# Kernel tuning notes

Measured on AMD Instinct MI355X. Metric: run time of the kernel, lower is better.

## Reference

```python
import jax, jax.numpy as jnp
import numpy as np

B, C_IN, H_IMG, W_IMG = 8, 3, 512, 512
PATCH, EMBED, HEADS = 16, 768, 8
N = (H_IMG // PATCH) * (W_IMG // PATCH)  # 1024 patches per branch
OUT_DIM = H_IMG * W_IMG * C_IN // (N * 2)  # 384


def conv2d(x, w, b, stride):
    y = jax.lax.conv_general_dilated(x, w, (stride, stride), 'VALID',
                                     dimension_numbers=('NCHW', 'OIHW', 'NCHW'))
    return y + b[None, :, None, None]


def maxpool2(x):
    return jax.lax.reduce_window(x, -jnp.inf, jax.lax.max, (1, 1, 2, 2), (1, 1, 2, 2), 'VALID')


def patch_embed(x, w, b, pos):
    # conv stride=patch -> (B, E, H/p, W/p) -> (B, N, E) + pos
    y = conv2d(x, w, b, PATCH)
    Bc, E, Hp, Wp = y.shape
    return y.reshape(Bc, E, Hp * Wp).transpose(0, 2, 1) + pos


def bilinear_up_ac(x, s):
    # bilinear upsample, align_corners=True, separable along H then W
    Bc, Cc, H, W = x.shape
    ys = jnp.linspace(0.0, H - 1.0, H * s)
    y0 = jnp.floor(ys).astype(jnp.int32)
    y1 = jnp.minimum(y0 + 1, H - 1)
    wy = (ys - y0.astype(x.dtype))[:, None]  # (Ho,1)
    xh = x[:, :, y0, :] * (1.0 - wy) + x[:, :, y1, :] * wy
    xs = jnp.linspace(0.0, W - 1.0, W * s)
    x0 = jnp.floor(xs).astype(jnp.int32)
    x1 = jnp.minimum(x0 + 1, W - 1)
    wx = xs - x0.astype(x.dtype)
    return xh[:, :, :, x0] * (1.0 - wx) + xh[:, :, :, x1] * wx


def setup_inputs() -> dict:
    key = jax.random.key(0)
    ks = jax.random.split(key, 13)
    std = 0.02
    return {
        'img': jax.random.normal(ks[0], (B, C_IN, H_IMG, W_IMG), jnp.float32),
        'context': jax.random.normal(ks[1], (B, C_IN, 2 * H_IMG, 2 * W_IMG), jnp.float32),
        'patch_w': jax.random.normal(ks[2], (EMBED, C_IN, PATCH, PATCH), jnp.float32) * std,
        'patch_b': jax.random.normal(ks[3], (EMBED,), jnp.float32) * std,
        'pos1': jax.random.normal(ks[4], (1, N, EMBED), jnp.float32) * std,
        'ctx_w': jax.random.normal(ks[5], (EMBED, C_IN, PATCH, PATCH), jnp.float32) * std,
        'ctx_b': jax.random.normal(ks[6], (EMBED,), jnp.float32) * std,
        'pos2': jax.random.normal(ks[7], (1, N, EMBED), jnp.float32) * std,
        'qkv_w': jax.random.normal(ks[8], (EMBED, 3 * EMBED), jnp.float32) * std,
        'proj_w': jax.random.normal(ks[9], (EMBED, OUT_DIM), jnp.float32) * std,
        'proj_b': jax.random.normal(ks[10], (OUT_DIM,), jnp.float32) * std,
        'up_w': jax.random.normal(ks[11], (C_IN, C_IN, 1, 1), jnp.float32) * std,
        'up_b': jax.random.normal(ks[12], (C_IN,), jnp.float32) * std,
    }


def reference(img, context, patch_w, patch_b, pos1, ctx_w, ctx_b, pos2,
              qkv_w, proj_w, proj_b, up_w, up_b):
    # patch embeddings
    x = patch_embed(img, patch_w, patch_b, pos1)                    # (B, N, E)
    ce = patch_embed(maxpool2(context), ctx_w, ctx_b, pos2)          # (B, N, E)
    # cross attention (naive, faithful to torch module incl. scale quirk)
    xc = jnp.concatenate([x, ce], axis=1)                            # (B, 2N, E)
    qkv = xc @ qkv_w                                                 # (B, 2N, 3E)
    hd2 = 2 * EMBED // HEADS                                         # 192 per head
    qkv = qkv.reshape(B, N, 3, HEADS, hd2).transpose(2, 0, 3, 1, 4)  # (3, B, H, N, 192)
    q, k, v = qkv[0], qkv[1], qkv[2]
    scale = (EMBED // HEADS) ** -0.5                                 # 96**-0.5 quirk
    attn = jax.nn.softmax(jnp.einsum('bhnd,bhmd->bhnm', q, k) * scale, axis=-1)
    o = jnp.einsum('bhnm,bhmd->bhnd', attn, v)                       # (B, H, N, 192)
    o = o.transpose(0, 2, 1, 3).reshape(B, 2 * N, EMBED)
    o = o @ proj_w + proj_b                                          # (B, 2N, 384)
    # reshape to image, 1x1 conv, bilinear x2 (align_corners), sigmoid, gate
    y = o.reshape(B, C_IN, H_IMG, W_IMG)
    y = conv2d(y, up_w, up_b, 1)
    y = jax.nn.sigmoid(bilinear_up_ac(y, 2))
    y = y * context
    return (y, attn)
```

## Files before the change

### kernel.cpp

```cpp
#include <hip/hip_runtime.h>
#include <math.h>


namespace {

typedef unsigned short u16;
typedef __attribute__((ext_vector_type(8))) __bf16 bf16x8;
typedef __attribute__((ext_vector_type(4))) float f32x4;

constexpr float SCALE = 0.10206207261596577f;

__device__ __forceinline__ u16 f2bf(float x) {
  unsigned u = __float_as_uint(x);
  return (u16)((u + 0x7FFFu + ((u >> 16) & 1u)) >> 16);
}

template <int BM, int BN>
__device__ __forceinline__ void mfma_core(const u16* __restrict__ A, int lda, int m0,
                                          const u16* __restrict__ B, int ldb, int n0,
                                          int K, u16* As, u16* Bs,
                                          f32x4 (&acc)[BM / 32][BN / 32]) {
  const int tid = threadIdx.x;
  const int lane = tid & 63, wid = tid >> 6;
  const int wr = wid >> 1, wc = wid & 1;
  const int fr = lane & 15, ks = lane >> 4;
  const int srow = lane >> 2, sslot = lane & 3;
  for (int kc = 0; kc < K; kc += 32) {
#pragma unroll
    for (int t = 0; t < BM / 64; ++t) {
      const int rb = (wid * (BM / 64) + t) * 16;
      const u16* src = A + (size_t)(m0 + rb + srow) * lda + kc + sslot * 8;
      __builtin_amdgcn_global_load_lds((const __attribute__((address_space(1))) void*)src,
                                       (__attribute__((address_space(3))) void*)(As + rb * 32),
                                       16, 0, 0);
    }
#pragma unroll
    for (int t = 0; t < BN / 64; ++t) {
      const int rb = (wid * (BN / 64) + t) * 16;
      const u16* src = B + (size_t)(n0 + rb + srow) * ldb + kc + sslot * 8;
      __builtin_amdgcn_global_load_lds((const __attribute__((address_space(1))) void*)src,
                                       (__attribute__((address_space(3))) void*)(Bs + rb * 32),
                                       16, 0, 0);
    }
    __syncthreads();
    bf16x8 a[BM / 32], b[BN / 32];
#pragma unroll
    for (int mi = 0; mi < BM / 32; ++mi)
      a[mi] = *(const bf16x8*)(As + (wr * (BM / 2) + mi * 16 + fr) * 32 + ks * 8);
#pragma unroll
    for (int ni = 0; ni < BN / 32; ++ni)
      b[ni] = *(const bf16x8*)(Bs + (wc * (BN / 2) + ni * 16 + fr) * 32 + ks * 8);
#pragma unroll
    for (int mi = 0; mi < BM / 32; ++mi)
#pragma unroll
      for (int ni = 0; ni < BN / 32; ++ni)
        acc[mi][ni] = __builtin_amdgcn_mfma_f32_16x16x32_bf16(a[mi], b[ni], acc[mi][ni], 0, 0, 0);
    __syncthreads();
  }
}


__global__ void cvt_bf16(const float* __restrict__ in, u16* __restrict__ out) {
  const int i = blockIdx.x * 256 + threadIdx.x;
  const float4 v = ((const float4*)in)[i];
  ((ushort4*)out)[i] = make_ushort4(f2bf(v.x), f2bf(v.y), f2bf(v.z), f2bf(v.w));
}

__global__ void cvt_t(const float* __restrict__ in, u16* __restrict__ out, int N, int K) {
  __shared__ float t[32][33];
  const int tx = threadIdx.x, ty = threadIdx.y;
  const int bn = blockIdx.x * 32, bk = blockIdx.y * 32;
#pragma unroll
  for (int i = 0; i < 4; ++i) t[ty * 4 + i][tx] = in[(size_t)(bk + ty * 4 + i) * N + bn + tx];
  __syncthreads();
#pragma unroll
  for (int i = 0; i < 4; ++i)
    out[(size_t)(bn + ty * 4 + i) * K + bk + tx] = f2bf(t[tx][ty * 4 + i]);
}


__global__ void im2col_img(const float* __restrict__ img, u16* __restrict__ A) {
  const int t = threadIdx.x;
  const int row = blockIdx.x;
  const int k4 = t * 4;
  const int c = k4 >> 8, rem = k4 & 255, i = rem >> 4, j = rem & 15;
  const int b = row >> 10, n = row & 1023;
  const int hp = n >> 5, wp = n & 31;
  const float4 v = *(const float4*)(img + ((size_t)(b * 3 + c) * 512 + hp * 16 + i) * 512 + wp * 16 + j);
  *(ushort4*)(A + (size_t)row * 768 + k4) = make_ushort4(f2bf(v.x), f2bf(v.y), f2bf(v.z), f2bf(v.w));
}

__global__ void im2col_ctx(const float* __restrict__ ctx, u16* __restrict__ A) {
  const int t = threadIdx.x;
  const int row = blockIdx.x;
  const int k4 = t * 4;
  const int c = k4 >> 8, rem = k4 & 255, i = rem >> 4, j = rem & 15;
  const int b = row >> 10, n = row & 1023;
  const int hp = n >> 5, wp = n & 31;
  const int y = hp * 16 + i, x = wp * 16 + j;
  const float* base = ctx + ((size_t)(b * 3 + c) * 1024 + 2 * y) * 1024 + 2 * x;
  const float4 r0a = *(const float4*)(base);
  const float4 r0b = *(const float4*)(base + 4);
  const float4 r1a = *(const float4*)(base + 1024);
  const float4 r1b = *(const float4*)(base + 1028);
  *(ushort4*)(A + (size_t)row * 768 + k4) = make_ushort4(
      f2bf(fmaxf(fmaxf(r0a.x, r0a.y), fmaxf(r1a.x, r1a.y))),
      f2bf(fmaxf(fmaxf(r0a.z, r0a.w), fmaxf(r1a.z, r1a.w))),
      f2bf(fmaxf(fmaxf(r0b.x, r0b.y), fmaxf(r1b.x, r1b.y))),
      f2bf(fmaxf(fmaxf(r0b.z, r0b.w), fmaxf(r1b.z, r1b.w))));
}


__global__ __launch_bounds__(256) void patch_gemm(
    const u16* __restrict__ A, const u16* __restrict__ W,
    const float* __restrict__ bias, const float* __restrict__ pos,
    u16* __restrict__ XC, int branch) {
  __shared__ u16 As[128 * 32], Bs[128 * 32];
  f32x4 acc[4][4];
#pragma unroll
  for (int mi = 0; mi < 4; ++mi)
#pragma unroll
    for (int ni = 0; ni < 4; ++ni) acc[mi][ni] = f32x4{0.f, 0.f, 0.f, 0.f};
  const int m0 = blockIdx.y * 128, n0 = blockIdx.x * 128;
  mfma_core<128, 128>(A, 768, m0, W, 768, n0, 768, As, Bs, acc);
  const int tid = threadIdx.x, lane = tid & 63, wid = tid >> 6;
  const int wr = wid >> 1, wc = wid & 1, fr = lane & 15, ks = lane >> 4;
#pragma unroll
  for (int mi = 0; mi < 4; ++mi)
#pragma unroll
    for (int j = 0; j < 4; ++j) {
      const int row = m0 + wr * 64 + mi * 16 + ks * 4 + j;
      const int b = row >> 10, n = row & 1023;
      u16* dst = XC + ((size_t)b * 2048 + branch * 1024 + n) * 768;
#pragma unroll
      for (int ni = 0; ni < 4; ++ni) {
        const int col = n0 + wc * 64 + ni * 16 + fr;
        dst[col] = f2bf(acc[mi][ni][j] + bias[col] + pos[(size_t)n * 768 + col]);
      }
    }
}

__global__ __launch_bounds__(256) void qkv_gemm(
    const u16* __restrict__ XC, const u16* __restrict__ Wt,
    u16* __restrict__ Qm, u16* __restrict__ Km, u16* __restrict__ Vt) {
  __shared__ u16 As[128 * 32], Bs[128 * 32];
  f32x4 acc[4][4];
#pragma unroll
  for (int mi = 0; mi < 4; ++mi)
#pragma unroll
    for (int ni = 0; ni < 4; ++ni) acc[mi][ni] = f32x4{0.f, 0.f, 0.f, 0.f};
  const int m0 = blockIdx.y * 128, n0 = blockIdx.x * 128;
  mfma_core<128, 128>(XC, 768, m0, Wt, 768, n0, 768, As, Bs, acc);
  const int tid = threadIdx.x, lane = tid & 63, wid = tid >> 6;
  const int wr = wid >> 1, wc = wid & 1, fr = lane & 15, ks = lane >> 4;
#pragma unroll
  for (int mi = 0; mi < 4; ++mi)
#pragma unroll
    for (int j = 0; j < 4; ++j) {
      const int row = m0 + wr * 64 + mi * 16 + ks * 4 + j;
      const int b = row >> 11, rl = row & 2047;
      const int n = rl >> 1, odd = rl & 1;
#pragma unroll
      for (int ni = 0; ni < 4; ++ni) {
        const int col = n0 + wc * 64 + ni * 16 + fr;
        const u16 v = f2bf(acc[mi][ni][j]);
        if (!odd) {
          if (col < 1536) {
            const int h = col / 192, d = col - h * 192;
            Qm[((size_t)(b * 8 + h) * 1024 + n) * 192 + d] = v;
          } else {
            const int c2 = col - 1536, h = c2 / 192, d = c2 - h * 192;
            Km[((size_t)(b * 8 + h) * 1024 + n) * 192 + d] = v;
          }
        } else {
          if (col < 768) {
            const int h = col / 192, d = col - h * 192;
            Km[((size_t)(b * 8 + 4 + h) * 1024 + n) * 192 + d] = v;
          } else {
            const int c2 = col - 768, h = c2 / 192, d = c2 - h * 192;
            Vt[((size_t)(b * 8 + h) * 192 + d) * 1024 + n] = v;
          }
        }
      }
    }
}

__global__ __launch_bounds__(256) void qk_gemm(
    const u16* __restrict__ Qm, const u16* __restrict__ Km, float* __restrict__ S) {
  __shared__ u16 As[128 * 32], Bs[128 * 32];
  f32x4 acc[4][4];
#pragma unroll
  for (int mi = 0; mi < 4; ++mi)
#pragma unroll
    for (int ni = 0; ni < 4; ++ni) acc[mi][ni] = f32x4{0.f, 0.f, 0.f, 0.f};
  const int bh = blockIdx.z;
  const int m0 = blockIdx.y * 128;
  const int n0 = blockIdx.x * 128;
  mfma_core<128, 128>(Qm + (size_t)bh * 196608, 192, m0, Km + (size_t)bh * 196608, 192, n0, 192,
                      As, Bs, acc);
  float* Sb = S + ((size_t)bh << 20);
  const int tid = threadIdx.x, lane = tid & 63, wid = tid >> 6;
  const int wr = wid >> 1, wc = wid & 1, fr = lane & 15, ks = lane >> 4;
#pragma unroll
  for (int mi = 0; mi < 4; ++mi)
#pragma unroll
    for (int j = 0; j < 4; ++j) {
      const int r = m0 + wr * 64 + mi * 16 + ks * 4 + j;
#pragma unroll
      for (int ni = 0; ni < 4; ++ni) {
        const int cc = n0 + wc * 64 + ni * 16 + fr;
        Sb[(size_t)r * 1024 + cc] = acc[mi][ni][j] * SCALE;
      }
    }
}

__global__ __launch_bounds__(256) void softmax_k(float* __restrict__ S, u16* __restrict__ Pbf) {
  __shared__ float red[8];
  float* p = S + ((size_t)blockIdx.x << 10);
  const int tid = threadIdx.x;
  float4 f = ((const float4*)p)[tid];
  float mx = fmaxf(fmaxf(f.x, f.y), fmaxf(f.z, f.w));
#pragma unroll
  for (int off = 32; off; off >>= 1) mx = fmaxf(mx, __shfl_xor(mx, off));
  if ((tid & 63) == 0) red[tid >> 6] = mx;
  __syncthreads();
  mx = fmaxf(fmaxf(red[0], red[1]), fmaxf(red[2], red[3]));
  const float e0 = expf(f.x - mx), e1 = expf(f.y - mx);
  const float e2 = expf(f.z - mx), e3 = expf(f.w - mx);
  float s = e0 + e1 + e2 + e3;
#pragma unroll
  for (int off = 32; off; off >>= 1) s += __shfl_xor(s, off);
  if ((tid & 63) == 0) red[4 + (tid >> 6)] = s;
  __syncthreads();
  const float inv = 1.0f / (red[4] + red[5] + red[6] + red[7]);
  const float o0 = e0 * inv, o1 = e1 * inv, o2 = e2 * inv, o3 = e3 * inv;
  ((float4*)p)[tid] = make_float4(o0, o1, o2, o3);
  *(ushort4*)(Pbf + ((size_t)blockIdx.x << 10) + tid * 4) =
      make_ushort4(f2bf(o0), f2bf(o1), f2bf(o2), f2bf(o3));
}

__global__ __launch_bounds__(256) void pv_gemm(
    const u16* __restrict__ Pbf, const u16* __restrict__ Vt, u16* __restrict__ O2) {
  __shared__ u16 As[128 * 32], Bs[192 * 32];
  f32x4 acc[4][6];
#pragma unroll
  for (int mi = 0; mi < 4; ++mi)
#pragma unroll
    for (int ni = 0; ni < 6; ++ni) acc[mi][ni] = f32x4{0.f, 0.f, 0.f, 0.f};
  const int bh = blockIdx.z;
  const int m0 = blockIdx.y * 128;
  mfma_core<128, 192>(Pbf + ((size_t)bh << 20), 1024, m0, Vt + (size_t)bh * 196608, 1024, 0, 1024,
                      As, Bs, acc);
  const int b = bh >> 3, h = bh & 7;
  const int tid = threadIdx.x, lane = tid & 63, wid = tid >> 6;
  const int wr = wid >> 1, wc = wid & 1, fr = lane & 15, ks = lane >> 4;
#pragma unroll
  for (int mi = 0; mi < 4; ++mi)
#pragma unroll
    for (int j = 0; j < 4; ++j) {
      const int n = m0 + wr * 64 + mi * 16 + ks * 4 + j;
      const int r = 2 * n + (h >> 2);
#pragma unroll
      for (int ni = 0; ni < 6; ++ni) {
        const int d = wc * 96 + ni * 16 + fr;
        O2[((size_t)b * 2048 + r) * 768 + (h & 3) * 192 + d] = f2bf(acc[mi][ni][j]);
      }
    }
}

__global__ __launch_bounds__(256) void proj_gemm(
    const u16* __restrict__ O2, const u16* __restrict__ Wt,
    const float* __restrict__ bias, float* __restrict__ P) {
  __shared__ u16 As[128 * 32], Bs[128 * 32];
  f32x4 acc[4][4];
#pragma unroll
  for (int mi = 0; mi < 4; ++mi)
#pragma unroll
    for (int ni = 0; ni < 4; ++ni) acc[mi][ni] = f32x4{0.f, 0.f, 0.f, 0.f};
  const int m0 = blockIdx.y * 128, n0 = blockIdx.x * 128;
  mfma_core<128, 128>(O2, 768, m0, Wt, 768, n0, 768, As, Bs, acc);
  const int tid = threadIdx.x, lane = tid & 63, wid = tid >> 6;
  const int wr = wid >> 1, wc = wid & 1, fr = lane & 15, ks = lane >> 4;
#pragma unroll
  for (int mi = 0; mi < 4; ++mi)
#pragma unroll
    for (int j = 0; j < 4; ++j) {
      const int row = m0 + wr * 64 + mi * 16 + ks * 4 + j;
#pragma unroll
      for (int ni = 0; ni < 4; ++ni) {
        const int col = n0 + wc * 64 + ni * 16 + fr;
        P[(size_t)row * 384 + col] = acc[mi][ni][j] + bias[col];
      }
    }
}

__global__ __launch_bounds__(256) void final_up(
    const float* __restrict__ P, const float* __restrict__ ctx,
    const float* __restrict__ up_w, const float* __restrict__ up_b,
    float* __restrict__ outY) {
  const size_t idx = (size_t)blockIdx.x * 256 + threadIdx.x;
  const int ow = (int)(idx & 1023);
  const int oh = (int)((idx >> 10) & 1023);
  const int b = (int)(idx >> 20);
  const float rr = 511.0f / 1023.0f;
  const float fy = oh * rr;
  const int y0 = (int)fy;
  const int y1 = y0 < 511 ? y0 + 1 : 511;
  const float wy = fy - (float)y0;
  const float fx = ow * rr;
  const int x0 = (int)fx;
  const int x1 = x0 < 511 ? x0 + 1 : 511;
  const float wx = fx - (float)x0;
  const float* Pb = P + (size_t)b * 786432;
  float v[3];
#pragma unroll
  for (int ci = 0; ci < 3; ++ci) {
    const float* pc = Pb + ci * 262144;
    const float a00 = pc[y0 * 512 + x0], a01 = pc[y0 * 512 + x1];
    const float a10 = pc[y1 * 512 + x0], a11 = pc[y1 * 512 + x1];
    v[ci] = (a00 * (1.f - wx) + a01 * wx) * (1.f - wy) +
            (a10 * (1.f - wx) + a11 * wx) * wy;
  }
#pragma unroll
  for (int co = 0; co < 3; ++co) {
    float u = up_b[co];
#pragma unroll
    for (int ci = 0; ci < 3; ++ci) u = fmaf(up_w[co * 3 + ci], v[ci], u);
    const float sg = 1.0f / (1.0f + expf(-u));
    const size_t o = (((size_t)b * 3 + co) << 20) + ((size_t)oh << 10) + ow;
    outY[o] = sg * ctx[o];
  }
}

}

extern "C" void kernel_launch(void* const* d_in, const int* in_sizes, int n_in,
                              void* d_out, int out_size, void* d_ws, size_t ws_size,
                              hipStream_t stream) {
  const float* img = (const float*)d_in[0];
  const float* ctx = (const float*)d_in[1];
  const float* patch_w = (const float*)d_in[2];
  const float* patch_b = (const float*)d_in[3];
  const float* pos1 = (const float*)d_in[4];
  const float* ctx_w = (const float*)d_in[5];
  const float* ctx_b = (const float*)d_in[6];
  const float* pos2 = (const float*)d_in[7];
  const float* qkv_w = (const float*)d_in[8];
  const float* proj_w = (const float*)d_in[9];
  const float* proj_b = (const float*)d_in[10];
  const float* up_w = (const float*)d_in[11];
  const float* up_b = (const float*)d_in[12];

  char* wsb = (char*)d_ws;
  u16* Pbf  = (u16*)(wsb);
  u16* Aimg = (u16*)(wsb);
  u16* Actx = (u16*)(wsb + 12582912);
  u16* XC   = (u16*)(wsb + 25165824);
  u16* Qm   = (u16*)(wsb + 50331648);
  u16* Km   = (u16*)(wsb + 75497472);
  u16* Vt   = (u16*)(wsb + 134217728);
  u16* O2   = (u16*)(wsb + 159383552);
  float* P  = (float*)(wsb + 184549376);
  u16* Wpat = (u16*)(wsb + 209715200);
  u16* Wctx = (u16*)(wsb + 210894848);
  u16* Wqt  = (u16*)(wsb + 212074496);
  u16* Wpt  = (u16*)(wsb + 215613440);

  float* outY = (float*)d_out;
  float* outA = (float*)d_out + 25165824;

  cvt_bf16<<<576, 256, 0, stream>>>(patch_w, Wpat);
  cvt_bf16<<<576, 256, 0, stream>>>(ctx_w, Wctx);
  cvt_t<<<dim3(72, 24), dim3(32, 8), 0, stream>>>(qkv_w, Wqt, 2304, 768);
  cvt_t<<<dim3(12, 24), dim3(32, 8), 0, stream>>>(proj_w, Wpt, 384, 768);
  im2col_img<<<8192, 192, 0, stream>>>(img, Aimg);
  im2col_ctx<<<8192, 192, 0, stream>>>(ctx, Actx);
  patch_gemm<<<dim3(6, 64), 256, 0, stream>>>(Aimg, Wpat, patch_b, pos1, XC, 0);
  patch_gemm<<<dim3(6, 64), 256, 0, stream>>>(Actx, Wctx, ctx_b, pos2, XC, 1);
  qkv_gemm<<<dim3(18, 128), 256, 0, stream>>>(XC, Wqt, Qm, Km, Vt);
  qk_gemm<<<dim3(8, 8, 64), 256, 0, stream>>>(Qm, Km, outA);
  softmax_k<<<65536, 256, 0, stream>>>(outA, Pbf);
  pv_gemm<<<dim3(1, 8, 64), 256, 0, stream>>>(Pbf, Vt, O2);
  proj_gemm<<<dim3(3, 128), 256, 0, stream>>>(O2, Wpt, proj_b, P);
  final_up<<<32768, 256, 0, stream>>>(P, ctx, up_w, up_b, outY);
}
```

Measured before the change: 919.9 us.

## Fuse QK, softmax and PV into one attention kernel; stage V transpose through LDS

Replaces the separate QK GEMM, softmax and PV GEMM kernels with a single kernel per 16-row query chunk. It computes full score rows in registers, does the softmax there, writes the fp32 attention output once, and runs PV from a bf16 P tile held in LDS. This removes the fp32 score round-trip (a write, a read and a rewrite of a 256MB buffer) and the bf16 P buffer. The qkv epilogue now transposes V through a shared-memory tile to get coalesced 16-byte stores, and final_up handles two pixels per thread with float2 accesses. The trade-off is that each block reloads all of K and V for only 16 query rows, which means much more redundant K/V traffic, and the new kernel is limited to a small number of waves per block.

New measurement: 2.720 ms. 196% more time.

```diff
diff --git a/kernel.cpp b/kernel.cpp
--- a/kernel.cpp
+++ b/kernel.cpp
@@ -144,6 +144,7 @@
     const u16* __restrict__ XC, const u16* __restrict__ Wt,
     u16* __restrict__ Qm, u16* __restrict__ Km, u16* __restrict__ Vt) {
   __shared__ u16 As[128 * 32], Bs[128 * 32];
+  __shared__ u16 vtile[128][72];
   f32x4 acc[4][4];
 #pragma unroll
   for (int mi = 0; mi < 4; ++mi)
@@ -153,12 +154,15 @@
   mfma_core<128, 128>(XC, 768, m0, Wt, 768, n0, 768, As, Bs, acc);
   const int tid = threadIdx.x, lane = tid & 63, wid = tid >> 6;
   const int wr = wid >> 1, wc = wid & 1, fr = lane & 15, ks = lane >> 4;
+  const bool hasV = (n0 >= 768);
+  const int bq = m0 >> 11;
+  const int nbase = (m0 & 2047) >> 1;
 #pragma unroll
   for (int mi = 0; mi < 4; ++mi)
 #pragma unroll
     for (int j = 0; j < 4; ++j) {
       const int row = m0 + wr * 64 + mi * 16 + ks * 4 + j;
-      const int b = row >> 11, rl = row & 2047;
+      const int rl = row & 2047;
       const int n = rl >> 1, odd = rl & 1;
 #pragma unroll
       for (int ni = 0; ni < 4; ++ni) {
@@ -167,104 +171,192 @@
         if (!odd) {
           if (col < 1536) {
             const int h = col / 192, d = col - h * 192;
-            Qm[((size_t)(b * 8 + h) * 1024 + n) * 192 + d] = v;
+            Qm[((size_t)(bq * 8 + h) * 1024 + n) * 192 + d] = v;
           } else {
             const int c2 = col - 1536, h = c2 / 192, d = c2 - h * 192;
-            Km[((size_t)(b * 8 + h) * 1024 + n) * 192 + d] = v;
+            Km[((size_t)(bq * 8 + h) * 1024 + n) * 192 + d] = v;
           }
+        } else if (hasV) {
+          vtile[col - n0][n - nbase] = v;
         } else {
-          if (col < 768) {
-            const int h = col / 192, d = col - h * 192;
-            Km[((size_t)(b * 8 + 4 + h) * 1024 + n) * 192 + d] = v;
-          } else {
-            const int c2 = col - 768, h = c2 / 192, d = c2 - h * 192;
-            Vt[((size_t)(b * 8 + h) * 192 + d) * 1024 + n] = v;
-          }
+          const int h = col / 192, d = col - h * 192;
+          Km[((size_t)(bq * 8 + 4 + h) * 1024 + n) * 192 + d] = v;
         }
       }
     }
-}
-
-__global__ __launch_bounds__(256) void qk_gemm(
-    const u16* __restrict__ Qm, const u16* __restrict__ Km, float* __restrict__ S) {
-  __shared__ u16 As[128 * 32], Bs[128 * 32];
-  f32x4 acc[4][4];
-#pragma unroll
-  for (int mi = 0; mi < 4; ++mi)
-#pragma unroll
-    for (int ni = 0; ni < 4; ++ni) acc[mi][ni] = f32x4{0.f, 0.f, 0.f, 0.f};
-  const int bh = blockIdx.z;
-  const int m0 = blockIdx.y * 128;
-  const int n0 = blockIdx.x * 128;
-  mfma_core<128, 128>(Qm + (size_t)bh * 196608, 192, m0, Km + (size_t)bh * 196608, 192, n0, 192,
-                      As, Bs, acc);
-  float* Sb = S + ((size_t)bh << 20);
-  const int tid = threadIdx.x, lane = tid & 63, wid = tid >> 6;
-  const int wr = wid >> 1, wc = wid & 1, fr = lane & 15, ks = lane >> 4;
-#pragma unroll
-  for (int mi = 0; mi < 4; ++mi)
-#pragma unroll
-    for (int j = 0; j < 4; ++j) {
-      const int r = m0 + wr * 64 + mi * 16 + ks * 4 + j;
-#pragma unroll
-      for (int ni = 0; ni < 4; ++ni) {
-        const int cc = n0 + wc * 64 + ni * 16 + fr;
-        Sb[(size_t)r * 1024 + cc] = acc[mi][ni][j] * SCALE;
-      }
-    }
-}
-
-__global__ __launch_bounds__(256) void softmax_k(float* __restrict__ S, u16* __restrict__ Pbf) {
-  __shared__ float red[8];
-  float* p = S + ((size_t)blockIdx.x << 10);
-  const int tid = threadIdx.x;
-  float4 f = ((const float4*)p)[tid];
-  float mx = fmaxf(fmaxf(f.x, f.y), fmaxf(f.z, f.w));
-#pragma unroll
-  for (int off = 32; off; off >>= 1) mx = fmaxf(mx, __shfl_xor(mx, off));
-  if ((tid & 63) == 0) red[tid >> 6] = mx;
-  __syncthreads();
-  mx = fmaxf(fmaxf(red[0], red[1]), fmaxf(red[2], red[3]));
-  const float e0 = expf(f.x - mx), e1 = expf(f.y - mx);
-  const float e2 = expf(f.z - mx), e3 = expf(f.w - mx);
-  float s = e0 + e1 + e2 + e3;
-#pragma unroll
-  for (int off = 32; off; off >>= 1) s += __shfl_xor(s, off);
-  if ((tid & 63) == 0) red[4 + (tid >> 6)] = s;
-  __syncthreads();
-  const float inv = 1.0f / (red[4] + red[5] + red[6] + red[7]);
-  const float o0 = e0 * inv, o1 = e1 * inv, o2 = e2 * inv, o3 = e3 * inv;
-  ((float4*)p)[tid] = make_float4(o0, o1, o2, o3);
-  *(ushort4*)(Pbf + ((size_t)blockIdx.x << 10) + tid * 4) =
-      make_ushort4(f2bf(o0), f2bf(o1), f2bf(o2), f2bf(o3));
-}
-
-__global__ __launch_bounds__(256) void pv_gemm(
-    const u16* __restrict__ Pbf, const u16* __restrict__ Vt, u16* __restrict__ O2) {
-  __shared__ u16 As[128 * 32], Bs[192 * 32];
-  f32x4 acc[4][6];
-#pragma unroll
-  for (int mi = 0; mi < 4; ++mi)
-#pragma unroll
-    for (int ni = 0; ni < 6; ++ni) acc[mi][ni] = f32x4{0.f, 0.f, 0.f, 0.f};
-  const int bh = blockIdx.z;
-  const int m0 = blockIdx.y * 128;
-  mfma_core<128, 192>(Pbf + ((size_t)bh << 20), 1024, m0, Vt + (size_t)bh * 196608, 1024, 0, 1024,
-                      As, Bs, acc);
+  if (hasV) {
+    __syncthreads();
+#pragma unroll
+    for (int t = 0; t < 4; ++t) {
+      const int slot = t * 256 + tid;
+      const int dloc = slot >> 3, m = slot & 7;
+      const int dglob = n0 - 768 + dloc;
+      const int h = dglob / 192, dd = dglob - h * 192;
+      *(uint4*)(Vt + ((size_t)(bq * 8 + h) * 192 + dd) * 1024 + nbase + m * 8) =
+          *(const uint4*)(&vtile[dloc][m * 8]);
+    }
+  }
+}
+
+__global__ __launch_bounds__(256) void attn_fused(
+    const u16* __restrict__ Qm, const u16* __restrict__ Km,
+    const u16* __restrict__ Vt, float* __restrict__ outA, u16* __restrict__ O2) {
+  const int rc = blockIdx.x;
+  const int bh = blockIdx.y;
   const int b = bh >> 3, h = bh & 7;
   const int tid = threadIdx.x, lane = tid & 63, wid = tid >> 6;
-  const int wr = wid >> 1, wc = wid & 1, fr = lane & 15, ks = lane >> 4;
-#pragma unroll
-  for (int mi = 0; mi < 4; ++mi)
+  const int fr = lane & 15, ks = lane >> 4;
+
+  const u16* Q = Qm + (size_t)bh * 196608;
+  const u16* K = Km + (size_t)bh * 196608;
+  const u16* V = Vt + (size_t)bh * 196608;
+  float* Sb = outA + ((size_t)bh << 20);
+
+  __shared__ u16 KV[12288];
+  __shared__ u16 P_lds[32 * 16 * 32];
+  __shared__ float red[16][4];
+
+  bf16x8 qa[6];
+  {
+    const u16* qrow = Q + (size_t)(rc * 16 + fr) * 192 + ks * 8;
+#pragma unroll
+    for (int kc = 0; kc < 6; ++kc) qa[kc] = *(const bf16x8*)(qrow + kc * 32);
+  }
+
+  f32x4 acc[8][2];
+#pragma unroll
+  for (int nc = 0; nc < 8; ++nc)
+#pragma unroll
+    for (int ti = 0; ti < 2; ++ti) acc[nc][ti] = f32x4{0.f, 0.f, 0.f, 0.f};
+
+  for (int nc = 0; nc < 8; ++nc) {
+#pragma unroll 1
+    for (int half = 0; half < 2; ++half) {
+#pragma unroll
+      for (int t = 0; t < 6; ++t) {
+        const int kcl = t >> 1;
+        const int r = ((t & 1) << 8) + tid;
+        const int krow = r >> 2, m = r & 3;
+        const u16* src = K + (size_t)(nc * 128 + krow) * 192 + half * 96 + kcl * 32 + m * 8;
+        __builtin_amdgcn_global_load_lds((const __attribute__((address_space(1))) void*)src,
+                                         (__attribute__((address_space(3))) void*)(KV + (t * 256 + tid) * 8),
+                                         16, 0, 0);
+      }
+      __syncthreads();
+#pragma unroll
+      for (int kcl = 0; kcl < 3; ++kcl) {
+        const bf16x8 aq = qa[half * 3 + kcl];
+#pragma unroll
+        for (int ti = 0; ti < 2; ++ti) {
+          const bf16x8 bk = *(const bf16x8*)(KV + (kcl * 128 + wid * 32 + ti * 16 + fr) * 32 + ks * 8);
+          acc[nc][ti] = __builtin_amdgcn_mfma_f32_16x16x32_bf16(aq, bk, acc[nc][ti], 0, 0, 0);
+        }
+      }
+      __syncthreads();
+    }
+  }
+
+  float mj[4];
+#pragma unroll
+  for (int j = 0; j < 4; ++j) mj[j] = -3.4e38f;
+#pragma unroll
+  for (int nc = 0; nc < 8; ++nc)
+#pragma unroll
+    for (int ti = 0; ti < 2; ++ti)
+#pragma unroll
+      for (int j = 0; j < 4; ++j) mj[j] = fmaxf(mj[j], acc[nc][ti][j]);
+#pragma unroll
+  for (int w = 1; w <= 8; w <<= 1)
+#pragma unroll
+    for (int j = 0; j < 4; ++j) mj[j] = fmaxf(mj[j], __shfl_xor(mj[j], w));
+  if (fr == 0) {
+#pragma unroll
+    for (int j = 0; j < 4; ++j) red[ks * 4 + j][wid] = mj[j];
+  }
+  __syncthreads();
+  float rm[4];
+#pragma unroll
+  for (int j = 0; j < 4; ++j) {
+    const float4 q = *(const float4*)red[ks * 4 + j];
+    rm[j] = fmaxf(fmaxf(q.x, q.y), fmaxf(q.z, q.w));
+  }
+  __syncthreads();
+  float sj[4] = {0.f, 0.f, 0.f, 0.f};
+#pragma unroll
+  for (int nc = 0; nc < 8; ++nc)
+#pragma unroll
+    for (int ti = 0; ti < 2; ++ti)
+#pragma unroll
+      for (int j = 0; j < 4; ++j) {
+        const float p = expf((acc[nc][ti][j] - rm[j]) * SCALE);
+        acc[nc][ti][j] = p;
+        sj[j] += p;
+      }
+#pragma unroll
+  for (int w = 1; w <= 8; w <<= 1)
+#pragma unroll
+    for (int j = 0; j < 4; ++j) sj[j] += __shfl_xor(sj[j], w);
+  if (fr == 0) {
+#pragma unroll
+    for (int j = 0; j < 4; ++j) red[ks * 4 + j][wid] = sj[j];
+  }
+  __syncthreads();
+  float inv[4];
+#pragma unroll
+  for (int j = 0; j < 4; ++j) {
+    const float4 q = *(const float4*)red[ks * 4 + j];
+    inv[j] = 1.0f / (q.x + q.y + q.z + q.w);
+  }
+#pragma unroll
+  for (int nc = 0; nc < 8; ++nc)
+#pragma unroll
+    for (int ti = 0; ti < 2; ++ti)
+#pragma unroll
+      for (int j = 0; j < 4; ++j) {
+        const float pn = acc[nc][ti][j] * inv[j];
+        const int row = ks * 4 + j;
+        const int col = nc * 128 + wid * 32 + ti * 16 + fr;
+        Sb[(size_t)(rc * 16 + row) * 1024 + col] = pn;
+        P_lds[(((col >> 5) * 16) + row) * 32 + (col & 31)] = f2bf(pn);
+      }
+  __syncthreads();
+
+  f32x4 oacc[3];
+#pragma unroll
+  for (int ti = 0; ti < 3; ++ti) oacc[ti] = f32x4{0.f, 0.f, 0.f, 0.f};
+#pragma unroll 1
+  for (int kp = 0; kp < 16; ++kp) {
+#pragma unroll
+    for (int t = 0; t < 6; ++t) {
+      const int kcl = t / 3;
+      const int r = (t - kcl * 3) * 256 + tid;
+      const int d = r >> 2, m = r & 3;
+      const u16* src = V + (size_t)d * 1024 + kp * 64 + kcl * 32 + m * 8;
+      __builtin_amdgcn_global_load_lds((const __attribute__((address_space(1))) void*)src,
+                                       (__attribute__((address_space(3))) void*)(KV + (t * 256 + tid) * 8),
+                                       16, 0, 0);
+    }
+    __syncthreads();
+#pragma unroll
+    for (int kcl = 0; kcl < 2; ++kcl) {
+      const bf16x8 pa = *(const bf16x8*)(P_lds + ((kp * 2 + kcl) * 16 + fr) * 32 + ks * 8);
+#pragma unroll
+      for (int ti = 0; ti < 3; ++ti) {
+        const bf16x8 bv = *(const bf16x8*)(KV + (kcl * 192 + wid * 48 + ti * 16 + fr) * 32 + ks * 8);
+        oacc[ti] = __builtin_amdgcn_mfma_f32_16x16x32_bf16(pa, bv, oacc[ti], 0, 0, 0);
+      }
+    }
+    __syncthreads();
+  }
+
+#pragma unroll
+  for (int ti = 0; ti < 3; ++ti)
 #pragma unroll
     for (int j = 0; j < 4; ++j) {
-      const int n = m0 + wr * 64 + mi * 16 + ks * 4 + j;
-      const int r = 2 * n + (h >> 2);
-#pragma unroll
-      for (int ni = 0; ni < 6; ++ni) {
-        const int d = wc * 96 + ni * 16 + fr;
-        O2[((size_t)b * 2048 + r) * 768 + (h & 3) * 192 + d] = f2bf(acc[mi][ni][j]);
-      }
+      const int n = rc * 16 + ks * 4 + j;
+      const int r2 = 2 * n + (h >> 2);
+      const int d = wid * 48 + ti * 16 + fr;
+      O2[((size_t)b * 2048 + r2) * 768 + (h & 3) * 192 + d] = f2bf(oacc[ti][j]);
     }
 }
 
@@ -299,36 +391,46 @@
     const float* __restrict__ up_w, const float* __restrict__ up_b,
     float* __restrict__ outY) {
   const size_t idx = (size_t)blockIdx.x * 256 + threadIdx.x;
-  const int ow = (int)(idx & 1023);
-  const int oh = (int)((idx >> 10) & 1023);
-  const int b = (int)(idx >> 20);
+  const int owp = (int)(idx & 511);
+  const int oh = (int)((idx >> 9) & 1023);
+  const int b = (int)(idx >> 19);
   const float rr = 511.0f / 1023.0f;
   const float fy = oh * rr;
   const int y0 = (int)fy;
   const int y1 = y0 < 511 ? y0 + 1 : 511;
   const float wy = fy - (float)y0;
-  const float fx = ow * rr;
-  const int x0 = (int)fx;
-  const int x1 = x0 < 511 ? x0 + 1 : 511;
-  const float wx = fx - (float)x0;
   const float* Pb = P + (size_t)b * 786432;
-  float v[3];
-#pragma unroll
-  for (int ci = 0; ci < 3; ++ci) {
-    const float* pc = Pb + ci * 262144;
-    const float a00 = pc[y0 * 512 + x0], a01 = pc[y0 * 512 + x1];
-    const float a10 = pc[y1 * 512 + x0], a11 = pc[y1 * 512 + x1];
-    v[ci] = (a00 * (1.f - wx) + a01 * wx) * (1.f - wy) +
-            (a10 * (1.f - wx) + a11 * wx) * wy;
+  float v[2][3];
+#pragma unroll
+  for (int px = 0; px < 2; ++px) {
+    const int ow = owp * 2 + px;
+    const float fx = ow * rr;
+    const int x0 = (int)fx;
+    const int x1 = x0 < 511 ? x0 + 1 : 511;
+    const float wx = fx - (float)x0;
+#pragma unroll
+    for (int ci = 0; ci < 3; ++ci) {
+      const float* pc = Pb + ci * 262144;
+      const float a00 = pc[y0 * 512 + x0], a01 = pc[y0 * 512 + x1];
+      const float a10 = pc[y1 * 512 + x0], a11 = pc[y1 * 512 + x1];
+      v[px][ci] = (a00 * (1.f - wx) + a01 * wx) * (1.f - wy) +
+                  (a10 * (1.f - wx) + a11 * wx) * wy;
+    }
   }
 #pragma unroll
   for (int co = 0; co < 3; ++co) {
-    float u = up_b[co];
-#pragma unroll
-    for (int ci = 0; ci < 3; ++ci) u = fmaf(up_w[co * 3 + ci], v[ci], u);
-    const float sg = 1.0f / (1.0f + expf(-u));
-    const size_t o = (((size_t)b * 3 + co) << 20) + ((size_t)oh << 10) + ow;
-    outY[o] = sg * ctx[o];
+    const size_t o = (((size_t)b * 3 + co) << 20) + ((size_t)oh << 10) + owp * 2;
+    const float2 c2 = *(const float2*)(ctx + o);
+    float2 res;
+#pragma unroll
+    for (int px = 0; px < 2; ++px) {
+      float u = up_b[co];
+#pragma unroll
+      for (int ci = 0; ci < 3; ++ci) u = fmaf(up_w[co * 3 + ci], v[px][ci], u);
+      const float sg = 1.0f / (1.0f + expf(-u));
+      if (px == 0) res.x = sg * c2.x; else res.y = sg * c2.y;
+    }
+    *(float2*)(outY + o) = res;
   }
 }
 
@@ -352,7 +454,6 @@
   const float* up_b = (const float*)d_in[12];
 
   char* wsb = (char*)d_ws;
-  u16* Pbf  = (u16*)(wsb);
   u16* Aimg = (u16*)(wsb);
   u16* Actx = (u16*)(wsb + 12582912);
   u16* XC   = (u16*)(wsb + 25165824);
@@ -378,9 +479,7 @@
   patch_gemm<<<dim3(6, 64), 256, 0, stream>>>(Aimg, Wpat, patch_b, pos1, XC, 0);
   patch_gemm<<<dim3(6, 64), 256, 0, stream>>>(Actx, Wctx, ctx_b, pos2, XC, 1);
   qkv_gemm<<<dim3(18, 128), 256, 0, stream>>>(XC, Wqt, Qm, Km, Vt);
-  qk_gemm<<<dim3(8, 8, 64), 256, 0, stream>>>(Qm, Km, outA);
-  softmax_k<<<65536, 256, 0, stream>>>(outA, Pbf);
-  pv_gemm<<<dim3(1, 8, 64), 256, 0, stream>>>(Pbf, Vt, O2);
+  attn_fused<<<dim3(64, 64), 256, 0, stream>>>(Qm, Km, Vt, outA, O2);
   proj_gemm<<<dim3(3, 128), 256, 0, stream>>>(O2, Wpt, proj_b, P);
-  final_up<<<32768, 256, 0, stream>>>(P, ctx, up_w, up_b, outY);
-}
+  final_up<<<16384, 256, 0, stream>>>(P, ctx, up_w, up_b, outY);
+}
```
